# Performance work log

Hardware: AMD Instinct MI355X
Metric: run time of the kernel (lower is better)

Reference implementation:

```python
import jax, jax.numpy as jnp
import numpy as np

N_NODES = 50000
N_EDGES = 800000
IN_CH = 64
HID = 128
LAST_HID = 256


def setup_inputs() -> dict:
    key = jax.random.key(0)
    ks = jax.random.split(key, 12)
    x = jax.random.normal(ks[0], (N_NODES, IN_CH), dtype=jnp.float32)
    edge_index = jax.random.randint(ks[1], (2, N_EDGES), 0, N_NODES, dtype=jnp.int64)
    s = lambda fan_in: 1.0 / np.sqrt(fan_in)
    return {
        "x": x,
        "edge_index": edge_index,
        # SAGEConv1: lin_l (aggregated neighbors, with bias), lin_r (root, no bias)
        "W1l": jax.random.normal(ks[2], (HID, IN_CH), dtype=jnp.float32) * s(IN_CH),
        "b1l": jnp.zeros((HID,), dtype=jnp.float32),
        "W1r": jax.random.normal(ks[3], (HID, IN_CH), dtype=jnp.float32) * s(IN_CH),
        # SAGEConv2 -> 1 channel
        "W2l": jax.random.normal(ks[4], (1, HID), dtype=jnp.float32) * s(HID),
        "b2l": jnp.zeros((1,), dtype=jnp.float32),
        "W2r": jax.random.normal(ks[5], (1, HID), dtype=jnp.float32) * s(HID),
        # fc1 (LazyLinear bound to N_NODES input features) and fc2
        "fc1_W": jax.random.normal(ks[6], (LAST_HID, N_NODES), dtype=jnp.float32) * s(N_NODES),
        "fc1_b": jnp.zeros((LAST_HID,), dtype=jnp.float32),
        "fc2_W": jax.random.normal(ks[7], (1, LAST_HID), dtype=jnp.float32) * s(LAST_HID),
        "fc2_b": jnp.zeros((1,), dtype=jnp.float32),
    }


def _sage_conv(h, src, dst, Wl, bl, Wr, n_nodes):
    # PyG SAGEConv (mean aggr): out = lin_l(mean_{j in N(i)} x_j) + lin_r(x_i)
    msgs = h[src]  # [E, F] gather of source node features
    summed = jax.ops.segment_sum(msgs, dst, num_segments=n_nodes)  # [N, F]
    deg = jax.ops.segment_sum(jnp.ones((src.shape[0],), h.dtype), dst, num_segments=n_nodes)
    agg = summed / jnp.maximum(deg, 1.0)[:, None]
    return agg @ Wl.T + bl + h @ Wr.T


def reference(x, edge_index, W1l, b1l, W1r, W2l, b2l, W2r, fc1_W, fc1_b, fc2_W, fc2_b):
    n = x.shape[0]
    src, dst = edge_index[0], edge_index[1]
    h = jax.nn.relu(_sage_conv(x, src, dst, W1l, b1l, W1r, n))   # [N, HID]
    h = jax.nn.relu(_sage_conv(h, src, dst, W2l, b2l, W2r, n))   # [N, 1]
    v = h[:, 0]                                                   # [N]
    z = fc1_W @ v + fc1_b                                         # [LAST_HID]
    pred = fc2_W @ z + fc2_b                                      # [1]
    return pred[0]  # scalar (torch.squeeze)
```

## Files before the change

### kernel.cpp

```cpp
#include <hip/hip_runtime.h>

#define N_NODESC 50000
#define N_EDGESC 800000
#define MAXDEG 64

__global__ void k0_init(int* __restrict__ deg, float* __restrict__ z) {
    int i = blockIdx.x * 256 + threadIdx.x;
    if (i < N_NODESC) deg[i] = 0;
    if (i < 256) z[i] = 0.0f;
}

#define K1_BLOCKS 2048
#define K1_EPB (N_EDGESC / (K1_BLOCKS / 8))
__global__ void k1_bucket(const int* __restrict__ ei, int* __restrict__ deg,
                          int* __restrict__ bucket) {
    int g   = blockIdx.x & 7;
    int idx = blockIdx.x >> 3;
    int lo = g * (N_NODESC / 8), hi = lo + (N_NODESC / 8);
    int e0 = idx * K1_EPB;
    for (int i = threadIdx.x; i < K1_EPB; i += 256) {
        int e = e0 + i;
        int dst = ei[N_EDGESC + e];
        int src = ei[e];
        if (dst >= lo && dst < hi) {
            int slot = atomicAdd(&deg[dst], 1);
            if (slot < MAXDEG) bucket[dst * MAXDEG + slot] = src;
        }
    }
}

__global__ void k2_agg(const float* __restrict__ x, const int* __restrict__ deg,
                       const int* __restrict__ bucket, float* __restrict__ agg) {
    int lane = threadIdx.x & 63;
    int node = blockIdx.x * 4 + (threadIdx.x >> 6);
    int g  = lane >> 4;
    int c4 = lane & 15;
    int d = deg[node];
    int c = min(d, MAXDEG);
    int bidx = bucket[node * MAXDEG + lane];
    float4 acc = make_float4(0.f, 0.f, 0.f, 0.f);
    for (int k = 0; k < c; k += 8) {
        int i0 = k + g, i1 = k + 4 + g;
        int b0 = __shfl(bidx, i0);
        int b1 = __shfl(bidx, i1);
        if (i0 < c) {
            float4 v = ((const float4*)(x + b0 * 64))[c4];
            acc.x += v.x; acc.y += v.y; acc.z += v.z; acc.w += v.w;
        }
        if (i1 < c) {
            float4 v = ((const float4*)(x + b1 * 64))[c4];
            acc.x += v.x; acc.y += v.y; acc.z += v.z; acc.w += v.w;
        }
    }
    #pragma unroll
    for (int m = 16; m <= 32; m <<= 1) {
        acc.x += __shfl_xor(acc.x, m);
        acc.y += __shfl_xor(acc.y, m);
        acc.z += __shfl_xor(acc.z, m);
        acc.w += __shfl_xor(acc.w, m);
    }
    if (g == 0) {
        float inv = 1.0f / (float)max(d, 1);
        ((float4*)(agg + node * 64))[c4] =
            make_float4(acc.x * inv, acc.y * inv, acc.z * inv, acc.w * inv);
    }
}

#define WS 68

__launch_bounds__(256, 2)
__global__ void k3_mm_fused(const float* __restrict__ x, const float* __restrict__ agg,
                            const float* __restrict__ W1l, const float* __restrict__ b1l,
                            const float* __restrict__ W1r,
                            const float* __restrict__ W2l, const float* __restrict__ W2r,
                            float* __restrict__ s_out, float* __restrict__ t_out) {
    __shared__ __align__(16) float sW[128 * WS];
    __shared__ __align__(16) float sXA[128 * WS];
    __shared__ float sB[128], sL[128], sR[128];

    int tid = threadIdx.x;
    int tx = tid & 15;
    int ty = tid >> 4;
    int node0 = blockIdx.x * 128;

    if (tid < 128) { sB[tid] = b1l[tid]; sL[tid] = W2l[tid]; sR[tid] = W2r[tid]; }

    float acc[8][8];
    #pragma unroll
    for (int i = 0; i < 8; i++)
        #pragma unroll
        for (int j = 0; j < 8; j++) acc[i][j] = 0.f;

    for (int ph = 0; ph < 2; ph++) {
        const float* Wsrc = (ph == 0) ? W1r : W1l;
        const float* Asrc = (ph == 0) ? x : agg;
        __syncthreads();
        #pragma unroll
        for (int i = tid * 4; i < 128 * 64; i += 1024) {
            float4 w = *(const float4*)(Wsrc + i);
            int o = i >> 6, k = i & 63;
            *(float4*)&sW[o * WS + k] = w;
        }
        #pragma unroll
        for (int i = tid * 4; i < 128 * 64; i += 1024) {
            int n = i >> 6, k = i & 63;
            int node = node0 + n;
            float4 a = make_float4(0.f, 0.f, 0.f, 0.f);
            if (node < N_NODESC) a = *(const float4*)(Asrc + node * 64 + k);
            *(float4*)&sXA[n * WS + k] = a;
        }
        __syncthreads();
        for (int k = 0; k < 64; k += 4) {
            float4 a4[8], w4[8];
            #pragma unroll
            for (int ni = 0; ni < 8; ni++)
                a4[ni] = *(const float4*)&sXA[(ty + 16 * ni) * WS + k];
            #pragma unroll
            for (int oj = 0; oj < 8; oj++)
                w4[oj] = *(const float4*)&sW[(tx + 16 * oj) * WS + k];
            #pragma unroll
            for (int ni = 0; ni < 8; ni++)
                #pragma unroll
                for (int oj = 0; oj < 8; oj++)
                    acc[ni][oj] += a4[ni].x * w4[oj].x + a4[ni].y * w4[oj].y
                                 + a4[ni].z * w4[oj].z + a4[ni].w * w4[oj].w;
        }
    }

    #pragma unroll
    for (int ni = 0; ni < 8; ni++) {
        float sp = 0.f, tp = 0.f;
        #pragma unroll
        for (int oj = 0; oj < 8; oj++) {
            int o = tx + 16 * oj;
            float h = fmaxf(acc[ni][oj] + sB[o], 0.f);
            sp += h * sL[o];
            tp += h * sR[o];
        }
        #pragma unroll
        for (int m = 1; m <= 8; m <<= 1) {
            sp += __shfl_xor(sp, m);
            tp += __shfl_xor(tp, m);
        }
        if (tx == 0) {
            int node = node0 + ty + 16 * ni;
            if (node < N_NODESC) { s_out[node] = sp; t_out[node] = tp; }
        }
    }
}

__global__ void k4_layer2(const float* __restrict__ s, const float* __restrict__ t,
                          const int* __restrict__ deg, const int* __restrict__ bucket,
                          const float* __restrict__ b2l, float* __restrict__ v) {
    int tid = threadIdx.x;
    int lane = tid & 15;
    int node = blockIdx.x * 16 + (tid >> 4);
    int d = deg[node];
    int c = min(d, MAXDEG);
    float sum = 0.f;
    for (int k = lane; k < c; k += 16) sum += s[bucket[node * MAXDEG + k]];
    sum += __shfl_xor(sum, 1);
    sum += __shfl_xor(sum, 2);
    sum += __shfl_xor(sum, 4);
    sum += __shfl_xor(sum, 8);
    if (lane == 0) {
        float h = sum / (float)max(d, 1) + b2l[0] + t[node];
        v[node] = fmaxf(h, 0.f);
    }
}

__global__ void k5_fc1(const float* __restrict__ fc1W, const float* __restrict__ v,
                       float* __restrict__ z) {
    int row = blockIdx.x >> 2;
    int part = blockIdx.x & 3;
    const float4* W4 = (const float4*)(fc1W + row * 50000 + part * 12500);
    const float4* v4 = (const float4*)(v + part * 12500);
    float sum = 0.f;
    for (int i = threadIdx.x; i < 3125; i += 256) {
        float4 w = W4[i], a = v4[i];
        sum += w.x * a.x + w.y * a.y + w.z * a.z + w.w * a.w;
    }
    #pragma unroll
    for (int m = 1; m < 64; m <<= 1) sum += __shfl_xor(sum, m);
    __shared__ float red[4];
    if ((threadIdx.x & 63) == 0) red[threadIdx.x >> 6] = sum;
    __syncthreads();
    if (threadIdx.x == 0) atomicAdd(&z[row], red[0] + red[1] + red[2] + red[3]);
}

__global__ void k6_head(const float* __restrict__ z, const float* __restrict__ fc1b,
                        const float* __restrict__ fc2W, const float* __restrict__ fc2b,
                        float* __restrict__ out) {
    int t = threadIdx.x;
    float val = (z[t] + fc1b[t]) * fc2W[t];
    #pragma unroll
    for (int m = 1; m < 64; m <<= 1) val += __shfl_xor(val, m);
    __shared__ float red[4];
    if ((t & 63) == 0) red[t >> 6] = val;
    __syncthreads();
    if (t == 0) out[0] = red[0] + red[1] + red[2] + red[3] + fc2b[0];
}

extern "C" void kernel_launch(void* const* d_in, const int* in_sizes, int n_in,
                              void* d_out, int out_size, void* d_ws, size_t ws_size,
                              hipStream_t stream) {
    const float* x    = (const float*)d_in[0];
    const int*   ei   = (const int*)d_in[1];
    const float* W1l  = (const float*)d_in[2];
    const float* b1l  = (const float*)d_in[3];
    const float* W1r  = (const float*)d_in[4];
    const float* W2l  = (const float*)d_in[5];
    const float* b2l  = (const float*)d_in[6];
    const float* W2r  = (const float*)d_in[7];
    const float* fc1W = (const float*)d_in[8];
    const float* fc1b = (const float*)d_in[9];
    const float* fc2W = (const float*)d_in[10];
    const float* fc2b = (const float*)d_in[11];
    float* out = (float*)d_out;

    char* ws = (char*)d_ws;
    int*   deg    = (int*)  (ws + 0);
    float* z      = (float*)(ws + 200192);
    int*   bucket = (int*)  (ws + 201216);
    float* agg    = (float*)(ws + 13001216);
    float* s      = (float*)(ws + 25801216);
    float* t      = (float*)(ws + 26001216);
    float* v      = (float*)(ws + 26201216);

    k0_init   <<<196,   256, 0, stream>>>(deg, z);
    k1_bucket <<<K1_BLOCKS, 256, 0, stream>>>(ei, deg, bucket);
    k2_agg    <<<12500, 256, 0, stream>>>(x, deg, bucket, agg);
    k3_mm_fused<<<391,  256, 0, stream>>>(x, agg, W1l, b1l, W1r, W2l, W2r, s, t);
    k4_layer2 <<<3125,  256, 0, stream>>>(s, t, deg, bucket, b2l, v);
    k5_fc1    <<<1024,  256, 0, stream>>>(fc1W, v, z);
    k6_head   <<<1,     256, 0, stream>>>(z, fc1b, fc2W, fc2b, out);
}
```

Measured before the change: 230.3 us.

## Run layer-1 GEMM on bf16 MFMA with hi/lo split-precision emulation

Replaces the FP32 FMA-based fused layer-1 matmul with a kernel using bf16 MFMA 16x16x32 instructions. Inputs and weights are each split into bf16 high and low parts, and three MFMAs per tile keep accuracy close to FP32. Weights are held in registers per wave, and the tile is 64 nodes per block, so the grid doubles to 782 blocks. The per-block W staging in LDS disappears, at the cost of extra conversion work and LDS atomics for the reduction.

```diff
diff --git a/kernel.cpp b/kernel.cpp
--- a/kernel.cpp
+++ b/kernel.cpp
@@ -3,6 +3,18 @@
 #define N_NODESC 50000
 #define N_EDGESC 800000
 #define MAXDEG 64
+
+typedef short bf16x8 __attribute__((ext_vector_type(8)));
+typedef float f32x4  __attribute__((ext_vector_type(4)));
+
+__device__ inline unsigned short f2bf(float f) {
+    unsigned u = __float_as_uint(f);
+    unsigned r = u + 0x7FFFu + ((u >> 16) & 1u);
+    return (unsigned short)(r >> 16);
+}
+__device__ inline float bf2f(unsigned short h) {
+    return __uint_as_float(((unsigned)h) << 16);
+}
 
 __global__ void k0_init(int* __restrict__ deg, float* __restrict__ z) {
     int i = blockIdx.x * 256 + threadIdx.x;
@@ -66,86 +78,133 @@
     }
 }
 
-#define WS 68
-
-__launch_bounds__(256, 2)
-__global__ void k3_mm_fused(const float* __restrict__ x, const float* __restrict__ agg,
-                            const float* __restrict__ W1l, const float* __restrict__ b1l,
-                            const float* __restrict__ W1r,
-                            const float* __restrict__ W2l, const float* __restrict__ W2r,
-                            float* __restrict__ s_out, float* __restrict__ t_out) {
-    __shared__ __align__(16) float sW[128 * WS];
-    __shared__ __align__(16) float sXA[128 * WS];
-    __shared__ float sB[128], sL[128], sR[128];
+#define K3S 144
+
+__launch_bounds__(256, 3)
+__global__ void k3_mm_mfma(const float* __restrict__ x, const float* __restrict__ agg,
+                           const float* __restrict__ W1l, const float* __restrict__ b1l,
+                           const float* __restrict__ W1r,
+                           const float* __restrict__ W2l, const float* __restrict__ W2r,
+                           float* __restrict__ s_out, float* __restrict__ t_out) {
+    __shared__ __align__(16) short sAhi[64 * K3S];
+    __shared__ __align__(16) short sAlo[64 * K3S];
+    __shared__ float sS[64], sT[64];
 
     int tid = threadIdx.x;
-    int tx = tid & 15;
-    int ty = tid >> 4;
-    int node0 = blockIdx.x * 128;
-
-    if (tid < 128) { sB[tid] = b1l[tid]; sL[tid] = W2l[tid]; sR[tid] = W2r[tid]; }
-
-    float acc[8][8];
-    #pragma unroll
-    for (int i = 0; i < 8; i++)
-        #pragma unroll
-        for (int j = 0; j < 8; j++) acc[i][j] = 0.f;
-
-    for (int ph = 0; ph < 2; ph++) {
-        const float* Wsrc = (ph == 0) ? W1r : W1l;
-        const float* Asrc = (ph == 0) ? x : agg;
-        __syncthreads();
-        #pragma unroll
-        for (int i = tid * 4; i < 128 * 64; i += 1024) {
-            float4 w = *(const float4*)(Wsrc + i);
-            int o = i >> 6, k = i & 63;
-            *(float4*)&sW[o * WS + k] = w;
-        }
-        #pragma unroll
-        for (int i = tid * 4; i < 128 * 64; i += 1024) {
-            int n = i >> 6, k = i & 63;
-            int node = node0 + n;
-            float4 a = make_float4(0.f, 0.f, 0.f, 0.f);
-            if (node < N_NODESC) a = *(const float4*)(Asrc + node * 64 + k);
-            *(float4*)&sXA[n * WS + k] = a;
-        }
-        __syncthreads();
-        for (int k = 0; k < 64; k += 4) {
-            float4 a4[8], w4[8];
-            #pragma unroll
-            for (int ni = 0; ni < 8; ni++)
-                a4[ni] = *(const float4*)&sXA[(ty + 16 * ni) * WS + k];
-            #pragma unroll
-            for (int oj = 0; oj < 8; oj++)
-                w4[oj] = *(const float4*)&sW[(tx + 16 * oj) * WS + k];
-            #pragma unroll
-            for (int ni = 0; ni < 8; ni++)
-                #pragma unroll
-                for (int oj = 0; oj < 8; oj++)
-                    acc[ni][oj] += a4[ni].x * w4[oj].x + a4[ni].y * w4[oj].y
-                                 + a4[ni].z * w4[oj].z + a4[ni].w * w4[oj].w;
-        }
-    }
-
-    #pragma unroll
-    for (int ni = 0; ni < 8; ni++) {
-        float sp = 0.f, tp = 0.f;
-        #pragma unroll
-        for (int oj = 0; oj < 8; oj++) {
-            int o = tx + 16 * oj;
-            float h = fmaxf(acc[ni][oj] + sB[o], 0.f);
-            sp += h * sL[o];
-            tp += h * sR[o];
-        }
-        #pragma unroll
-        for (int m = 1; m <= 8; m <<= 1) {
-            sp += __shfl_xor(sp, m);
-            tp += __shfl_xor(tp, m);
-        }
-        if (tx == 0) {
-            int node = node0 + ty + 16 * ni;
-            if (node < N_NODESC) { s_out[node] = sp; t_out[node] = tp; }
-        }
+    int lane = tid & 63;
+    int wave = tid >> 6;
+    int col = lane & 15;
+    int quad = lane >> 4;
+    int node0 = blockIdx.x * 64;
+
+    if (tid < 64) { sS[tid] = 0.f; sT[tid] = 0.f; }
+
+    int o_base = wave * 32;
+    bf16x8 bhi[2][4], blo[2][4];
+    float bias_r[2], w2l_r[2], w2r_r[2];
+    #pragma unroll
+    for (int oc = 0; oc < 2; oc++) {
+        int o = o_base + oc * 16 + col;
+        bias_r[oc] = b1l[o]; w2l_r[oc] = W2l[o]; w2r_r[oc] = W2r[o];
+        #pragma unroll
+        for (int ks = 0; ks < 4; ks++) {
+            int k0 = ks * 32 + quad * 8;
+            const float* wrow = (k0 < 64) ? (W1r + o * 64 + k0)
+                                          : (W1l + o * 64 + (k0 - 64));
+            #pragma unroll
+            for (int j = 0; j < 8; j++) {
+                float w = wrow[j];
+                unsigned short h = f2bf(w);
+                bhi[oc][ks][j] = (short)h;
+                blo[oc][ks][j] = (short)f2bf(w - bf2f(h));
+            }
+        }
+    }
+
+    #pragma unroll
+    for (int i = 0; i < 4; i++) {
+        int c = tid + 256 * i;
+        int n = c >> 4, kc = c & 15;
+        int node = node0 + n;
+        float v[8];
+        if (node < N_NODESC) {
+            const float* src = (kc < 8) ? (x + node * 64 + kc * 8)
+                                        : (agg + node * 64 + (kc - 8) * 8);
+            float4 v0 = *(const float4*)src;
+            float4 v1 = *(const float4*)(src + 4);
+            v[0] = v0.x; v[1] = v0.y; v[2] = v0.z; v[3] = v0.w;
+            v[4] = v1.x; v[5] = v1.y; v[6] = v1.z; v[7] = v1.w;
+        } else {
+            #pragma unroll
+            for (int j = 0; j < 8; j++) v[j] = 0.f;
+        }
+        bf16x8 hv, lv;
+        #pragma unroll
+        for (int j = 0; j < 8; j++) {
+            unsigned short h = f2bf(v[j]);
+            hv[j] = (short)h;
+            lv[j] = (short)f2bf(v[j] - bf2f(h));
+        }
+        *(bf16x8*)&sAhi[n * K3S + kc * 8] = hv;
+        *(bf16x8*)&sAlo[n * K3S + kc * 8] = lv;
+    }
+    __syncthreads();
+
+    f32x4 acc[4][2];
+    #pragma unroll
+    for (int nt = 0; nt < 4; nt++)
+        #pragma unroll
+        for (int oc = 0; oc < 2; oc++) acc[nt][oc] = (f32x4)0.f;
+
+    #pragma unroll
+    for (int ks = 0; ks < 4; ks++) {
+        #pragma unroll
+        for (int nt = 0; nt < 4; nt++) {
+            int off = (nt * 16 + col) * K3S + ks * 32 + quad * 8;
+            bf16x8 ah = *(const bf16x8*)&sAhi[off];
+            bf16x8 al = *(const bf16x8*)&sAlo[off];
+            #pragma unroll
+            for (int oc = 0; oc < 2; oc++) {
+                acc[nt][oc] = __builtin_amdgcn_mfma_f32_16x16x32_bf16(ah, bhi[oc][ks], acc[nt][oc], 0, 0, 0);
+                acc[nt][oc] = __builtin_amdgcn_mfma_f32_16x16x32_bf16(al, bhi[oc][ks], acc[nt][oc], 0, 0, 0);
+                acc[nt][oc] = __builtin_amdgcn_mfma_f32_16x16x32_bf16(ah, blo[oc][ks], acc[nt][oc], 0, 0, 0);
+            }
+        }
+    }
+
+    #pragma unroll
+    for (int nt = 0; nt < 4; nt++) {
+        float sp[4] = {0.f, 0.f, 0.f, 0.f};
+        float tp[4] = {0.f, 0.f, 0.f, 0.f};
+        #pragma unroll
+        for (int oc = 0; oc < 2; oc++)
+            #pragma unroll
+            for (int reg = 0; reg < 4; reg++) {
+                float h = fmaxf(acc[nt][oc][reg] + bias_r[oc], 0.f);
+                sp[reg] += h * w2l_r[oc];
+                tp[reg] += h * w2r_r[oc];
+            }
+        #pragma unroll
+        for (int reg = 0; reg < 4; reg++) {
+            #pragma unroll
+            for (int m = 1; m <= 8; m <<= 1) {
+                sp[reg] += __shfl_xor(sp[reg], m);
+                tp[reg] += __shfl_xor(tp[reg], m);
+            }
+        }
+        if (col == 0) {
+            int nn = nt * 16 + quad * 4;
+            #pragma unroll
+            for (int reg = 0; reg < 4; reg++) {
+                atomicAdd(&sS[nn + reg], sp[reg]);
+                atomicAdd(&sT[nn + reg], tp[reg]);
+            }
+        }
+    }
+    __syncthreads();
+    if (tid < 64) {
+        int node = node0 + tid;
+        if (node < N_NODESC) { s_out[node] = sS[tid]; t_out[node] = sT[tid]; }
     }
 }
 
@@ -230,7 +289,7 @@
     k0_init   <<<196,   256, 0, stream>>>(deg, z);
     k1_bucket <<<K1_BLOCKS, 256, 0, stream>>>(ei, deg, bucket);
     k2_agg    <<<12500, 256, 0, stream>>>(x, deg, bucket, agg);
-    k3_mm_fused<<<391,  256, 0, stream>>>(x, agg, W1l, b1l, W1r, W2l, W2r, s, t);
+    k3_mm_mfma<<<782,  256, 0, stream>>>(x, agg, W1l, b1l, W1r, W2l, W2r, s, t);
     k4_layer2 <<<3125,  256, 0, stream>>>(s, t, deg, bucket, b2l, v);
     k5_fc1    <<<1024,  256, 0, stream>>>(fc1W, v, z);
     k6_head   <<<1,     256, 0, stream>>>(z, fc1b, fc2W, fc2b, out);
```

After: 214.6 us. 6.8% less time.
